# Kernel tuning notes

Hardware: AMD Instinct MI355X
Metric: run time of the kernel (lower is better)

## Reference

```python
import jax, jax.numpy as jnp
import numpy as np

B, T, N = 512, 1024, 48


def setup_inputs() -> dict:
    key = jax.random.key(0)
    k1, k2, k3, k4 = jax.random.split(key, 4)
    potentials = jax.random.normal(k1, (B, T, N), dtype=jnp.float32)
    y_true = jax.random.randint(k2, (B, T), 0, N, dtype=jnp.int32)
    lengths = jax.random.randint(k3, (B,), 1, T + 1, dtype=jnp.int32)
    transitions = jax.random.normal(k4, (N, N), dtype=jnp.float32)
    return {"potentials": potentials, "y_true": y_true,
            "lengths": lengths, "transitions": transitions}


def _crf_log_likelihood(potentials, tags, lengths, trans):
    # potentials: [B,T,N], tags: [B,T] int, lengths: [B] int, trans: [N,N]
    Bv, Tv, Nv = potentials.shape
    t_idx = jnp.arange(Tv)

    # ---- numerator: score of the given tag sequence ----
    unary = jnp.take_along_axis(potentials, tags[..., None], axis=2)[..., 0]  # [B,T]
    unary_mask = (t_idx[None, :] < lengths[:, None]).astype(potentials.dtype)
    unary_score = jnp.sum(unary * unary_mask, axis=1)  # [B]

    trans_scores = trans[tags[:, :-1], tags[:, 1:]]  # [B,T-1]
    pair_mask = (t_idx[None, 1:] < lengths[:, None]).astype(potentials.dtype)
    binary_score = jnp.sum(trans_scores * pair_mask, axis=1)  # [B]
    seq_score = unary_score + binary_score

    # ---- log partition: forward algorithm with length masking ----
    alpha0 = potentials[:, 0, :]  # [B,N]
    pots_rest = jnp.transpose(potentials[:, 1:, :], (1, 0, 2))  # [T-1,B,N]
    valid = (t_idx[1:, None] < lengths[None, :])  # [T-1,B]

    def step(alpha, inp):
        pot_t, v = inp  # [B,N], [B]
        # logsumexp over previous state: alpha[b,i] + trans[i,j]
        new_alpha = jax.nn.logsumexp(alpha[:, :, None] + trans[None, :, :], axis=1) + pot_t
        alpha = jnp.where(v[:, None], new_alpha, alpha)
        return alpha, None

    alpha_final, _ = jax.lax.scan(step, alpha0, (pots_rest, valid))
    log_norm = jax.nn.logsumexp(alpha_final, axis=-1)  # [B]

    return seq_score - log_norm


def reference(potentials, y_true, lengths, transitions):
    ll = _crf_log_likelihood(potentials, y_true.astype(jnp.int32),
                             lengths.astype(jnp.int32), transitions)
    return -ll  # per-sample NLL, shape [B]
```

## Files before the change

### kernel.cpp

```cpp
#include <hip/hip_runtime.h>
#include <cstdint>
#include <cstddef>

constexpr int Bb = 512;
constexpr int Tt = 1024;
constexpr int Nn = 48;
constexpr int SG = 16;
constexpr int NG = Bb / SG;
constexpr int Cc = 64;
constexpr int Lc = Tt / Cc;
constexpr int Wb = 32;

typedef short bf16x8 __attribute__((ext_vector_type(8)));
typedef float f32x4  __attribute__((ext_vector_type(4)));
typedef unsigned int u32x4 __attribute__((ext_vector_type(4)));

__device__ __forceinline__ unsigned int bf16_rne(float x) {
    const unsigned int u = __float_as_uint(x);
    return ((u + 0x7FFFu + ((u >> 16) & 1u)) >> 16);
}
__device__ __forceinline__ unsigned int pack2(float lo, float hi) {
    return bf16_rne(lo) | (bf16_rne(hi) << 16);
}
__device__ __forceinline__ float safe_log(float x) {
    return __logf(fmaxf(x, 1e-30f));
}

#define GLD(dst, p) asm volatile("global_load_dwordx4 %0, %1, off" : "=&v"(dst) : "v"(p))
#define WAITP() do { asm volatile("s_waitcnt vmcnt(9)"); __builtin_amdgcn_sched_barrier(0); } while (0)

__attribute__((amdgpu_waves_per_eu(2, 2)))
__launch_bounds__(64)
__global__ void crf_fused(const float* __restrict__ pot,
                          const int*   __restrict__ ytrue,
                          const int*   __restrict__ lengths,
                          const float* __restrict__ trans,
                          float*       __restrict__ out)
{
    __shared__ float trans_lds[Nn * Nn];

    const int lane = threadIdx.x;
    const int ln   = lane & 15;
    const int q    = lane >> 4;
    const int gidx = blockIdx.x >> 6;
    const int c    = blockIdx.x & 63;
    const int s0   = gidx * SG;

    for (int i = lane; i < Nn * Nn; i += 64) trans_lds[i] = trans[i];
    __syncthreads();

    {
        const int    b    = blockIdx.x >> 2;
        const int    h    = blockIdx.x & 3;
        const int    lenb = lengths[b];
        const int*   yrow = ytrue + (size_t)b * Tt;
        const float* prow = pot + (size_t)b * Tt * Nn;
        float gold = 0.0f;
#pragma unroll
        for (int k = 0; k < Tt / 256; ++k) {
            const int   t    = h * (Tt / 4) + lane + 64 * k;
            const int   yt   = yrow[t];
            const int   ytm1 = yrow[(t > 0) ? (t - 1) : 0];
            const float u    = prow[(size_t)t * Nn + yt];
            const float tr   = trans_lds[ytm1 * Nn + yt];
            gold += (t < lenb) ? u : 0.0f;
            gold += (t >= 1 && t < lenb) ? tr : 0.0f;
        }
#pragma unroll
        for (int off = 32; off > 0; off >>= 1) gold += __shfl_xor(gold, off);
        if (lane == 0) atomicAdd(&out[b], -gold);
    }

    const int len_ln = lengths[s0 + ln];
    int lmax = len_ln;
#pragma unroll
    for (int off = 8; off > 0; off >>= 1) {
        const int o = __shfl_xor(lmax, off);
        lmax = (o > lmax) ? o : lmax;
    }

    const int start = (c == 0) ? 1 : c * Lc;
    if (c > 0 && start >= lmax) return;
    const int end = ((c + 1) * Lc < lmax) ? (c + 1) * Lc : lmax;

    bf16x8 Wf[3][2];
#pragma unroll
    for (int nt = 0; nt < 3; ++nt)
#pragma unroll
        for (int kc = 0; kc < 2; ++kc)
#pragma unroll
            for (int d = 0; d < 8; ++d) {
                int i;
                if (kc == 0) {
                    i = 16 * (d >> 2) + 4 * q + (d & 3);
                } else {
                    i = (q < 2) ? (32 + 8 * q + d) : -1;
                }
                const float v = (i >= 0) ? __expf(trans_lds[i * Nn + nt * 16 + ln]) : 0.0f;
                Wf[nt][kc][d] = (short)bf16_rne(v);
            }

    const int slA = ((2 * q) & 3) * 16 + ln;
    const int slB = slA + 16;
    const int slC = ln;

    const float* prow = pot + (size_t)(s0 + ln) * (Tt * Nn);
    const float* pp0 = prow + 0 * 16 + q * 4;
    const float* pp1 = prow + 1 * 16 + q * 4;
    const float* pp2 = prow + 2 * 16 + q * 4;

    int t0 = (c == 0) ? 1 : (start - Wb);
    if (t0 < 1) t0 = 1;

    f32x4 pin0 = *(const f32x4*)(pp0 + (size_t)(t0 - 1) * Nn);
    f32x4 pin1 = *(const f32x4*)(pp1 + (size_t)(t0 - 1) * Nn);
    f32x4 pin2 = *(const f32x4*)(pp2 + (size_t)(t0 - 1) * Nn);
    const float cb0 = __shfl(pin0[0], slC);

    float gacc = (c == 0) ? cb0 : 0.0f;
    f32x4 prev0, prev1, prev2;
#pragma unroll
    for (int r = 0; r < 4; ++r) {
        prev0[r] = __expf(pin0[r] - cb0);
        prev1[r] = __expf(pin1[r] - cb0);
        prev2[r] = __expf(pin2[r] - cb0);
    }

    unsigned int pk00 = pack2(prev0[0], prev0[1]);
    unsigned int pk01 = pack2(prev0[2], prev0[3]);
    unsigned int pk10 = pack2(prev1[0], prev1[1]);
    unsigned int pk11 = pack2(prev1[2], prev1[3]);
    unsigned int pk20 = pack2(prev2[0], prev2[1]);
    unsigned int pk21 = pack2(prev2[2], prev2[3]);
    bf16x8 Bf0 = __builtin_bit_cast(bf16x8, (u32x4){pk00, pk01, pk10, pk11});
    bf16x8 Bf1 = __builtin_bit_cast(bf16x8, (u32x4){
        (unsigned int)__shfl((int)pk20, slA), (unsigned int)__shfl((int)pk21, slA),
        (unsigned int)__shfl((int)pk20, slB), (unsigned int)__shfl((int)pk21, slB)});

    f32x4 P00, P01, P02, P10, P11, P12, P20, P21, P22, P30, P31, P32;
    {
        const size_t ta = (size_t)((t0 + 0 < Tt) ? t0 + 0 : Tt - 1) * Nn;
        const size_t tb = (size_t)((t0 + 1 < Tt) ? t0 + 1 : Tt - 1) * Nn;
        const size_t tc = (size_t)((t0 + 2 < Tt) ? t0 + 2 : Tt - 1) * Nn;
        const size_t td = (size_t)((t0 + 3 < Tt) ? t0 + 3 : Tt - 1) * Nn;
        const float* a;
        a = pp0 + ta; GLD(P00, a);  a = pp1 + ta; GLD(P01, a);  a = pp2 + ta; GLD(P02, a);
        a = pp0 + tb; GLD(P10, a);  a = pp1 + tb; GLD(P11, a);  a = pp2 + tb; GLD(P12, a);
        a = pp0 + tc; GLD(P20, a);  a = pp1 + tc; GLD(P21, a);  a = pp2 + tc; GLD(P22, a);
        a = pp0 + td; GLD(P30, a);  a = pp1 + td; GLD(P31, a);  a = pp2 + td; GLD(P32, a);
    }
    WAITP();
    f32x4 epv0, epv1, epv2;
#pragma unroll
    for (int r = 0; r < 4; ++r) {
        epv0[r] = __expf(P00[r]);
        epv1[r] = __expf(P01[r]);
        epv2[r] = __expf(P02[r]);
    }

    const int ksteps = ((end - t0) + 3) & ~3;

#define CRF_STEP(KK, LA0, LA1, LA2, NB0, NB1, NB2)                              \
    {                                                                           \
        const int t   = t0 + (KK);                                              \
        const size_t tld = (size_t)((t + 4 < Tt) ? (t + 4) : (Tt - 1)) * Nn;    \
        const float* pa_ = pp0 + tld;  GLD(LA0, pa_);                           \
        const float* pb_ = pp1 + tld;  GLD(LA1, pb_);                           \
        const float* pc_ = pp2 + tld;  GLD(LA2, pc_);                           \
        f32x4 z = {0.0f, 0.0f, 0.0f, 0.0f};                                     \
        f32x4 D0 = __builtin_amdgcn_mfma_f32_16x16x32_bf16(Wf[0][0], Bf0, z, 0, 0, 0); \
        f32x4 D1 = __builtin_amdgcn_mfma_f32_16x16x32_bf16(Wf[1][0], Bf0, z, 0, 0, 0); \
        f32x4 D2 = __builtin_amdgcn_mfma_f32_16x16x32_bf16(Wf[2][0], Bf0, z, 0, 0, 0); \
        D0 = __builtin_amdgcn_mfma_f32_16x16x32_bf16(Wf[0][1], Bf1, D0, 0, 0, 0); \
        D1 = __builtin_amdgcn_mfma_f32_16x16x32_bf16(Wf[1][1], Bf1, D1, 0, 0, 0); \
        D2 = __builtin_amdgcn_mfma_f32_16x16x32_bf16(Wf[2][1], Bf1, D2, 0, 0, 0); \
        f32x4 a0, a1, a2;                                                       \
        _Pragma("unroll")                                                       \
        for (int r = 0; r < 4; ++r) {                                           \
            a0[r] = D0[r] * epv0[r];                                            \
            a1[r] = D1[r] * epv1[r];                                            \
            a2[r] = D2[r] * epv2[r];                                            \
        }                                                                       \
        const float cb = __shfl(a0[0], slC);                                    \
        const float rr = __builtin_amdgcn_rcpf(fmaxf(cb, 1e-30f));              \
        const float lg = safe_log(cb);                                          \
        gacc += ((t >= start) && (t < end) && (t + 1 < len_ln)) ? lg : 0.0f;    \
        const bool act = (t < len_ln);                                          \
        _Pragma("unroll")                                                       \
        for (int r = 0; r < 4; ++r) {                                           \
            prev0[r] = act ? a0[r] : prev0[r];                                  \
            prev1[r] = act ? a1[r] : prev1[r];                                  \
            prev2[r] = act ? a2[r] : prev2[r];                                  \
        }                                                                       \
        pk00 = pack2(prev0[0], prev0[1]);                                       \
        pk01 = pack2(prev0[2], prev0[3]);                                       \
        pk10 = pack2(prev1[0], prev1[1]);                                       \
        pk11 = pack2(prev1[2], prev1[3]);                                       \
        pk20 = pack2(prev2[0], prev2[1]);                                       \
        pk21 = pack2(prev2[2], prev2[3]);                                       \
        Bf0 = __builtin_bit_cast(bf16x8, (u32x4){pk00, pk01, pk10, pk11});      \
        Bf1 = __builtin_bit_cast(bf16x8, (u32x4){                               \
            (unsigned int)__shfl((int)pk20, slA), (unsigned int)__shfl((int)pk21, slA), \
            (unsigned int)__shfl((int)pk20, slB), (unsigned int)__shfl((int)pk21, slB)}); \
        WAITP();                      \
        _Pragma("unroll")                                                       \
        for (int r = 0; r < 4; ++r) {                                           \
            epv0[r] = __expf(NB0[r]) * rr;                                      \
            epv1[r] = __expf(NB1[r]) * rr;                                      \
            epv2[r] = __expf(NB2[r]) * rr;                                      \
        }                                                                       \
    }

    for (int k = 0; k < ksteps; k += 4) {
        CRF_STEP(k + 0, P00, P01, P02, P10, P11, P12);
        CRF_STEP(k + 1, P10, P11, P12, P20, P21, P22);
        CRF_STEP(k + 2, P20, P21, P22, P30, P31, P32);
        CRF_STEP(k + 3, P30, P31, P32, P00, P01, P02);
    }
#undef CRF_STEP

    asm volatile("s_waitcnt vmcnt(0)");

    float rs = prev0[0] + prev0[1] + prev0[2] + prev0[3]
             + prev1[0] + prev1[1] + prev1[2] + prev1[3]
             + prev2[0] + prev2[1] + prev2[2] + prev2[3];
    rs += __shfl_xor(rs, 16);
    rs += __shfl_xor(rs, 32);

    const bool active_chunk = (c == 0) || (c * Lc < len_ln);
    const bool last = active_chunk && (len_ln <= (c + 1) * Lc);
    const float G = gacc + (last ? safe_log(rs) : 0.0f);
    if (lane < 16) atomicAdd(&out[s0 + ln], G);
}

extern "C" void kernel_launch(void* const* d_in, const int* in_sizes, int n_in,
                              void* d_out, int out_size, void* d_ws, size_t ws_size,
                              hipStream_t stream)
{
    const float* pot   = (const float*)d_in[0];
    const int*   ytrue = (const int*)  d_in[1];
    const int*   lens  = (const int*)  d_in[2];
    const float* trans = (const float*)d_in[3];
    float*       out   = (float*)d_out;

    hipMemsetAsync(out, 0, (size_t)out_size * sizeof(float), stream);
    crf_fused<<<dim3(NG * Cc), dim3(64), 0, stream>>>(pot, ytrue, lens, trans, out);
}
```

Measured before the change: 188.4 us.

## Stage potentials through LDS with async global_load_lds double-buffered ring

Replaces the per-lane register prefetch of potentials, which used explicit global_load_dwordx4 and a vmcnt wait, with direct global-to-LDS loads into a 4-slot ring covering all 16 sequences at once. Each step now reads its tile from LDS and computes exp of the potentials inline, scaled by the previous step's reciprocal. The intent is to cut VGPR pressure and drop the waves_per_eu pin, at the cost of extra LDS traffic and full vmcnt(0) waits every two steps. The LDS ring and the trans table share the same buffer, and the code relies on the __syncthreads before staging to keep them apart.

```diff
diff --git a/kernel.cpp b/kernel.cpp
--- a/kernel.cpp
+++ b/kernel.cpp
@@ -10,6 +10,7 @@
 constexpr int Cc = 64;
 constexpr int Lc = Tt / Cc;
 constexpr int Wb = 32;
+constexpr int TILE = 3328;
 
 typedef short bf16x8 __attribute__((ext_vector_type(8)));
 typedef float f32x4  __attribute__((ext_vector_type(4)));
@@ -25,11 +26,12 @@
 __device__ __forceinline__ float safe_log(float x) {
     return __logf(fmaxf(x, 1e-30f));
 }
-
-#define GLD(dst, p) asm volatile("global_load_dwordx4 %0, %1, off" : "=&v"(dst) : "v"(p))
-#define WAITP() do { asm volatile("s_waitcnt vmcnt(9)"); __builtin_amdgcn_sched_barrier(0); } while (0)
-
-__attribute__((amdgpu_waves_per_eu(2, 2)))
+__device__ __forceinline__ void gll16(const float* g, const char* l) {
+    __builtin_amdgcn_global_load_lds(
+        (const __attribute__((address_space(1))) void*)g,
+        (__attribute__((address_space(3))) void*)l, 16, 0, 0);
+}
+
 __launch_bounds__(64)
 __global__ void crf_fused(const float* __restrict__ pot,
                           const int*   __restrict__ ytrue,
@@ -37,7 +39,8 @@
                           const float* __restrict__ trans,
                           float*       __restrict__ out)
 {
-    __shared__ float trans_lds[Nn * Nn];
+    __shared__ __align__(16) char smem_c[4 * TILE];
+    float* trans_lds = (float*)smem_c;
 
     const int lane = threadIdx.x;
     const int ln   = lane & 15;
@@ -137,60 +140,71 @@
         (unsigned int)__shfl((int)pk20, slA), (unsigned int)__shfl((int)pk21, slA),
         (unsigned int)__shfl((int)pk20, slB), (unsigned int)__shfl((int)pk21, slB)});
 
-    f32x4 P00, P01, P02, P10, P11, P12, P20, P21, P22, P30, P31, P32;
-    {
-        const size_t ta = (size_t)((t0 + 0 < Tt) ? t0 + 0 : Tt - 1) * Nn;
-        const size_t tb = (size_t)((t0 + 1 < Tt) ? t0 + 1 : Tt - 1) * Nn;
-        const size_t tc = (size_t)((t0 + 2 < Tt) ? t0 + 2 : Tt - 1) * Nn;
-        const size_t td = (size_t)((t0 + 3 < Tt) ? t0 + 3 : Tt - 1) * Nn;
-        const float* a;
-        a = pp0 + ta; GLD(P00, a);  a = pp1 + ta; GLD(P01, a);  a = pp2 + ta; GLD(P02, a);
-        a = pp0 + tb; GLD(P10, a);  a = pp1 + tb; GLD(P11, a);  a = pp2 + tb; GLD(P12, a);
-        a = pp0 + tc; GLD(P20, a);  a = pp1 + tc; GLD(P21, a);  a = pp2 + tc; GLD(P22, a);
-        a = pp0 + td; GLD(P30, a);  a = pp1 + td; GLD(P31, a);  a = pp2 + td; GLD(P32, a);
-    }
-    WAITP();
-    f32x4 epv0, epv1, epv2;
-#pragma unroll
-    for (int r = 0; r < 4; ++r) {
-        epv0[r] = __expf(P00[r]);
-        epv1[r] = __expf(P01[r]);
-        epv2[r] = __expf(P02[r]);
-    }
+    const float* srcp[4];
+#pragma unroll
+    for (int i = 0; i < 4; ++i) {
+        int g = 64 * i + lane;
+        int s = g / 13;  if (s > 15) s = 15;
+        int cg = g % 13; if (cg > 11) cg = 11;
+        srcp[i] = pot + (size_t)(s0 + s) * (Tt * Nn) + 4 * cg;
+    }
+
+    __syncthreads();
+
+#define STAGE(tt, SLOT) do {                                                    \
+        const size_t toff_ = (size_t)(((tt) < Tt) ? (tt) : (Tt - 1)) * Nn;      \
+        char* lb_ = smem_c + (SLOT) * TILE;                                     \
+        gll16(srcp[0] + toff_, lb_);                                            \
+        gll16(srcp[1] + toff_, lb_ + 1024);                                     \
+        gll16(srcp[2] + toff_, lb_ + 2048);                                     \
+        if (lane < 16) gll16(srcp[3] + toff_, lb_ + 3072);                      \
+    } while (0)
+
+#define BOUNDARY(KK) do {                                                       \
+        asm volatile("s_waitcnt vmcnt(0)" ::: "memory");                        \
+        STAGE(t0 + (KK) + 2, ((KK) + 2) & 3);                                   \
+        STAGE(t0 + (KK) + 3, ((KK) + 3) & 3);                                   \
+    } while (0)
+
+    const int lnq13 = ln * 13 + q;
+    float rrp = 1.0f;
+
+    STAGE(t0 + 0, 0);
+    STAGE(t0 + 1, 1);
 
     const int ksteps = ((end - t0) + 3) & ~3;
 
-#define CRF_STEP(KK, LA0, LA1, LA2, NB0, NB1, NB2)                              \
+#define CRF_STEP(KK, SLOT)                                                      \
     {                                                                           \
-        const int t   = t0 + (KK);                                              \
-        const size_t tld = (size_t)((t + 4 < Tt) ? (t + 4) : (Tt - 1)) * Nn;    \
-        const float* pa_ = pp0 + tld;  GLD(LA0, pa_);                           \
-        const float* pb_ = pp1 + tld;  GLD(LA1, pb_);                           \
-        const float* pc_ = pp2 + tld;  GLD(LA2, pc_);                           \
-        f32x4 z = {0.0f, 0.0f, 0.0f, 0.0f};                                     \
-        f32x4 D0 = __builtin_amdgcn_mfma_f32_16x16x32_bf16(Wf[0][0], Bf0, z, 0, 0, 0); \
-        f32x4 D1 = __builtin_amdgcn_mfma_f32_16x16x32_bf16(Wf[1][0], Bf0, z, 0, 0, 0); \
-        f32x4 D2 = __builtin_amdgcn_mfma_f32_16x16x32_bf16(Wf[2][0], Bf0, z, 0, 0, 0); \
-        D0 = __builtin_amdgcn_mfma_f32_16x16x32_bf16(Wf[0][1], Bf1, D0, 0, 0, 0); \
-        D1 = __builtin_amdgcn_mfma_f32_16x16x32_bf16(Wf[1][1], Bf1, D1, 0, 0, 0); \
-        D2 = __builtin_amdgcn_mfma_f32_16x16x32_bf16(Wf[2][1], Bf1, D2, 0, 0, 0); \
-        f32x4 a0, a1, a2;                                                       \
+        const int t_ = t0 + (KK);                                               \
+        const f32x4* tp_ = (const f32x4*)(smem_c + (SLOT) * TILE);              \
+        const f32x4 PA_ = tp_[lnq13];                                           \
+        const f32x4 PB_ = tp_[lnq13 + 4];                                       \
+        const f32x4 PC_ = tp_[lnq13 + 8];                                       \
+        f32x4 z_ = {0.0f, 0.0f, 0.0f, 0.0f};                                    \
+        f32x4 D0_ = __builtin_amdgcn_mfma_f32_16x16x32_bf16(Wf[0][0], Bf0, z_, 0, 0, 0); \
+        f32x4 D1_ = __builtin_amdgcn_mfma_f32_16x16x32_bf16(Wf[1][0], Bf0, z_, 0, 0, 0); \
+        f32x4 D2_ = __builtin_amdgcn_mfma_f32_16x16x32_bf16(Wf[2][0], Bf0, z_, 0, 0, 0); \
+        D0_ = __builtin_amdgcn_mfma_f32_16x16x32_bf16(Wf[0][1], Bf1, D0_, 0, 0, 0); \
+        D1_ = __builtin_amdgcn_mfma_f32_16x16x32_bf16(Wf[1][1], Bf1, D1_, 0, 0, 0); \
+        D2_ = __builtin_amdgcn_mfma_f32_16x16x32_bf16(Wf[2][1], Bf1, D2_, 0, 0, 0); \
+        f32x4 a0_, a1_, a2_;                                                    \
         _Pragma("unroll")                                                       \
         for (int r = 0; r < 4; ++r) {                                           \
-            a0[r] = D0[r] * epv0[r];                                            \
-            a1[r] = D1[r] * epv1[r];                                            \
-            a2[r] = D2[r] * epv2[r];                                            \
+            a0_[r] = D0_[r] * (__expf(PA_[r]) * rrp);                           \
+            a1_[r] = D1_[r] * (__expf(PB_[r]) * rrp);                           \
+            a2_[r] = D2_[r] * (__expf(PC_[r]) * rrp);                           \
         }                                                                       \
-        const float cb = __shfl(a0[0], slC);                                    \
-        const float rr = __builtin_amdgcn_rcpf(fmaxf(cb, 1e-30f));              \
-        const float lg = safe_log(cb);                                          \
-        gacc += ((t >= start) && (t < end) && (t + 1 < len_ln)) ? lg : 0.0f;    \
-        const bool act = (t < len_ln);                                          \
+        const float cb_ = __shfl(a0_[0], slC);                                  \
+        const float rr_ = __builtin_amdgcn_rcpf(fmaxf(cb_, 1e-30f));            \
+        const float lg_ = safe_log(cb_);                                        \
+        gacc += ((t_ >= start) && (t_ < end) && (t_ + 1 < len_ln)) ? lg_ : 0.0f; \
+        const bool act_ = (t_ < len_ln);                                        \
         _Pragma("unroll")                                                       \
         for (int r = 0; r < 4; ++r) {                                           \
-            prev0[r] = act ? a0[r] : prev0[r];                                  \
-            prev1[r] = act ? a1[r] : prev1[r];                                  \
-            prev2[r] = act ? a2[r] : prev2[r];                                  \
+            prev0[r] = act_ ? a0_[r] : prev0[r];                                \
+            prev1[r] = act_ ? a1_[r] : prev1[r];                                \
+            prev2[r] = act_ ? a2_[r] : prev2[r];                                \
         }                                                                       \
         pk00 = pack2(prev0[0], prev0[1]);                                       \
         pk01 = pack2(prev0[2], prev0[3]);                                       \
@@ -202,24 +216,22 @@
         Bf1 = __builtin_bit_cast(bf16x8, (u32x4){                               \
             (unsigned int)__shfl((int)pk20, slA), (unsigned int)__shfl((int)pk21, slA), \
             (unsigned int)__shfl((int)pk20, slB), (unsigned int)__shfl((int)pk21, slB)}); \
-        WAITP();                      \
-        _Pragma("unroll")                                                       \
-        for (int r = 0; r < 4; ++r) {                                           \
-            epv0[r] = __expf(NB0[r]) * rr;                                      \
-            epv1[r] = __expf(NB1[r]) * rr;                                      \
-            epv2[r] = __expf(NB2[r]) * rr;                                      \
-        }                                                                       \
+        rrp = rr_;                                                              \
     }
 
     for (int k = 0; k < ksteps; k += 4) {
-        CRF_STEP(k + 0, P00, P01, P02, P10, P11, P12);
-        CRF_STEP(k + 1, P10, P11, P12, P20, P21, P22);
-        CRF_STEP(k + 2, P20, P21, P22, P30, P31, P32);
-        CRF_STEP(k + 3, P30, P31, P32, P00, P01, P02);
+        BOUNDARY(k);
+        CRF_STEP(k + 0, 0);
+        CRF_STEP(k + 1, 1);
+        BOUNDARY(k + 2);
+        CRF_STEP(k + 2, 2);
+        CRF_STEP(k + 3, 3);
     }
 #undef CRF_STEP
-
-    asm volatile("s_waitcnt vmcnt(0)");
+#undef BOUNDARY
+#undef STAGE
+
+    asm volatile("s_waitcnt vmcnt(0)" ::: "memory");
 
     float rs = prev0[0] + prev0[1] + prev0[2] + prev0[3]
              + prev1[0] + prev1[1] + prev1[2] + prev1[3]
```

Result: no change. 185.8 us (-1.4%).
